# Performance work log

Measured on AMD Instinct MI355X. Metric: run time of the kernel, lower is better.

Reference implementation:

```python
import jax, jax.numpy as jnp
import numpy as np

B, N, T, E = 8, 4096, 16, 65536
D, H, O = 768, 4, 256
PER_TURN = N // T
NEG = -1e30


def setup_inputs() -> dict:
    key = jax.random.key(0)
    k = jax.random.split(key, 10)
    x = jax.random.normal(k[0], (B, N, D), dtype=jnp.float32)
    # turns sorted within each graph: node i has turn i // PER_TURN
    turns = jnp.tile(jnp.repeat(jnp.arange(T, dtype=jnp.int32), PER_TURN)[None, :], (B, 1))
    # edges: dst uniform over nodes, src uniform over nodes with turn[src] <= turn[dst]
    dst = jax.random.randint(k[1], (B, E), 0, N, dtype=jnp.int32)
    bound = (dst // PER_TURN + 1) * PER_TURN
    u = jax.random.uniform(k[2], (B, E), dtype=jnp.float32)
    src = jnp.minimum((u * bound).astype(jnp.int32), bound - 1)
    edge_index = jnp.stack([src, dst], axis=1)  # [B, 2, E]
    W = jax.random.normal(k[3], (D, H * D), dtype=jnp.float32) * 0.02
    a_src = jax.random.normal(k[4], (H, D), dtype=jnp.float32) * 0.05
    a_dst = jax.random.normal(k[5], (H, D), dtype=jnp.float32) * 0.05
    b_gat = jnp.zeros((D,), jnp.float32)
    w_att = jax.random.normal(k[6], (D, 1), dtype=jnp.float32) * 0.05
    b_att = jnp.zeros((1,), jnp.float32)
    w_cls = jax.random.normal(k[7], (D, O), dtype=jnp.float32) * 0.05
    b_cls = jnp.zeros((O,), jnp.float32)
    return dict(x=x, edge_index=edge_index, turns=turns, W=W, a_src=a_src,
                a_dst=a_dst, b_gat=b_gat, w_att=w_att, b_att=b_att,
                w_cls=w_cls, b_cls=b_cls)


def _forward(x, edge_index, turns, W, a_src, a_dst, b_gat, w_att, b_att, w_cls, b_cls, n_turns):
    n = x.shape[1]
    h_heads, d = a_src.shape

    def graph_fn(args):
        xg, ei, tg = args
        src, dst = ei[0], ei[1]

        def step(xc, t):
            active = tg <= t                                  # subgraph node mask [N]
            h = (xc @ W).reshape(n, h_heads, d)               # [N,H,D] per-head projections
            asrc = jnp.einsum('nhd,hd->nh', h, a_src)         # [N,H]
            adst = jnp.einsum('nhd,hd->nh', h, a_dst)
            emask = tg[dst] == t                              # only edges into current turn
            e = jax.nn.leaky_relu(asrc[src] + adst[dst], 0.2)  # [E,H]
            e = jnp.where(emask[:, None], e, NEG)
            # PyG GATConv add_self_loops=True: self-loop on every subgraph node
            s = jax.nn.leaky_relu(asrc + adst, 0.2)           # [N,H]
            s = jnp.where(active[:, None], s, NEG)
            m = jnp.maximum(jax.ops.segment_max(e, dst, num_segments=n), s)
            m = jnp.where(m > NEG * 0.5, m, 0.0)              # safe max for empty segments
            ee = jnp.where(emask[:, None], jnp.exp(e - m[dst]), 0.0)   # [E,H]
            se = jnp.where(active[:, None], jnp.exp(s - m), 0.0)       # [N,H]
            denom = jax.ops.segment_sum(ee, dst, num_segments=n) + se  # [N,H]
            msg = jax.ops.segment_sum(ee[:, :, None] * h[src], dst, num_segments=n)
            out = (msg + se[:, :, None] * h) / jnp.where(denom > 0, denom, 1.0)[:, :, None]
            out = out.mean(axis=1) + b_gat                    # concat=False -> mean over heads
            xn = jnp.where(active[:, None], out, xc)          # write back into graph.x
            # GlobalAttention pooling over subgraph nodes
            gate = (xn @ w_att + b_att).squeeze(-1)           # [N]
            g = jax.nn.softmax(jnp.where(active, gate, NEG))
            pooled = g @ xn                                   # [D]
            return xn, pooled @ w_cls + b_cls                 # [O]

        _, outs = jax.lax.scan(step, xg, jnp.arange(n_turns))
        return outs                                           # [T,O]

    outs = jax.lax.map(graph_fn, (x, edge_index, turns))      # sequential over graphs
    return outs[:, :, None, :]                                # [B,T,1,O] like torch.stack nesting


def reference(x, edge_index, turns, W, a_src, a_dst, b_gat, w_att, b_att, w_cls, b_cls):
    n_turns = int(turns.max()) + 1
    return _forward(x, edge_index, turns, W, a_src, a_dst, b_gat, w_att, b_att,
                    w_cls, b_cls, n_turns)
```

## Files before the change

### kernel.cpp

```cpp
#include <hip/hip_runtime.h>

typedef __attribute__((ext_vector_type(8))) short short8;
typedef __attribute__((ext_vector_type(8))) unsigned short ushort8;
typedef __attribute__((ext_vector_type(4))) float f32x4;

__device__ __forceinline__ float b2f(unsigned short u){
  union { unsigned int i; float f; } v; v.i = ((unsigned int)u)<<16; return v.f;
}
__device__ __forceinline__ unsigned short f2b(float f){
  unsigned int x = __float_as_uint(f);
  return (unsigned short)((x + 0x7fffu + ((x>>16)&1u))>>16);
}

__device__ __forceinline__ void gload16(const unsigned short* g, unsigned short* l){
  __builtin_amdgcn_global_load_lds((const __attribute__((address_space(1))) unsigned int*)g,
                                   (__attribute__((address_space(3))) unsigned int*)l, 16, 0, 0);
}

__global__ __launch_bounds__(256) void k_zero(int* p){
  p[blockIdx.x*256 + threadIdx.x] = 0;
}

__global__ __launch_bounds__(256) void k_hist(const int* __restrict__ ei, int* __restrict__ cnt){
  int idx = blockIdx.x*256 + threadIdx.x;
  int b = idx>>16, e = idx&65535;
  int dst = ei[b*131072 + 65536 + e];
  atomicAdd(&cnt[b*4096 + dst], 1);
}

__global__ __launch_bounds__(1024) void k_scan(int* __restrict__ cnt, int* __restrict__ offs){
  int b = blockIdx.x, tid = threadIdx.x;
  __shared__ int sums[1024];
  int base = tid*4;
  int c0 = cnt[b*4096+base+0], c1 = cnt[b*4096+base+1];
  int c2 = cnt[b*4096+base+2], c3 = cnt[b*4096+base+3];
  int t1 = c0, t2 = c0+c1, t3 = c0+c1+c2, tot = t3+c3;
  sums[tid] = tot;
  __syncthreads();
  for (int off=1; off<1024; off<<=1){
    int add = (tid>=off) ? sums[tid-off] : 0;
    __syncthreads();
    sums[tid] += add;
    __syncthreads();
  }
  int eb = sums[tid] - tot;
  offs[b*4097+base+0] = eb;      offs[b*4097+base+1] = eb+t1;
  offs[b*4097+base+2] = eb+t2;   offs[b*4097+base+3] = eb+t3;
  cnt[b*4096+base+0] = eb;       cnt[b*4096+base+1] = eb+t1;
  cnt[b*4096+base+2] = eb+t2;    cnt[b*4096+base+3] = eb+t3;
  if (tid==1023) offs[b*4097+4096] = sums[1023];
}

__global__ __launch_bounds__(256) void k_scatter(const int* __restrict__ ei, int* __restrict__ cur,
                                                 int* __restrict__ ss){
  int idx = blockIdx.x*256 + threadIdx.x;
  int b = idx>>16, e = idx&65535;
  int src = ei[b*131072 + e];
  int dst = ei[b*131072 + 65536 + e];
  int pos = atomicAdd(&cur[b*4096 + dst], 1);
  ss[b*65536 + pos] = src;
}

__global__ __launch_bounds__(256) void k_vavd(const float* __restrict__ W, const float* __restrict__ a_src,
                                              const float* __restrict__ a_dst, float* __restrict__ vavd){
  int wid = blockIdx.x*4 + (threadIdx.x>>6);
  int lane = threadIdx.x & 63;
  int i = wid>>3, h8 = wid&7, h = h8&3;
  const float* a = (h8<4 ? a_src : a_dst) + h*768;
  const float* wrow = W + i*3072 + h*768;
  float acc = 0.f;
  #pragma unroll
  for (int j12=0; j12<12; j12++){ int j = lane + j12*64; acc += wrow[j]*a[j]; }
  #pragma unroll
  for (int d=1; d<64; d<<=1) acc += __shfl_xor(acc, d);
  if (lane==0) vavd[i*8 + h8] = acc;
}

__global__ __launch_bounds__(256) void k_prep_w(const float* __restrict__ W, unsigned short* __restrict__ wmT,
                                                unsigned short* __restrict__ wpT){
  int g = blockIdx.x*256 + threadIdx.x;
  int i = g%768, j = g/768;
  float s = 0.f;
  #pragma unroll
  for (int h=0; h<4; h++){
    float w = W[i*3072 + h*768 + j];
    s += w;
    wpT[j*3072 + h*768 + i] = f2b(w);
  }
  wmT[j*768 + i] = f2b(0.25f*s);
}

__global__ __launch_bounds__(256) void k_prep0(const float* __restrict__ x0, const float* __restrict__ vavd,
                                               float* __restrict__ ad0){
  int b = blockIdx.y;
  int node = blockIdx.x*4 + (threadIdx.x>>6);
  int lane = threadIdx.x & 63;
  size_t roff = (size_t)(b*4096 + node)*768;
  float acc[8];
  #pragma unroll
  for (int k=0;k<8;k++) acc[k]=0.f;
  #pragma unroll
  for (int j12=0; j12<12; j12++){
    int j = lane + j12*64;
    float xv = x0[roff + j];
    const float* vp = vavd + j*8;
    #pragma unroll
    for (int k=0;k<8;k++) acc[k]+=xv*vp[k];
  }
  #pragma unroll
  for (int k=0;k<8;k++){
    #pragma unroll
    for (int d=1; d<64; d<<=1) acc[k] += __shfl_xor(acc[k], d);
  }
  if (lane==0){
    float* o = ad0 + (size_t)(b*4096 + node)*8;
    #pragma unroll
    for (int k=0;k<8;k++) o[k]=acc[k];
  }
}

__global__ __launch_bounds__(256) void k_logits(const unsigned short* __restrict__ st,
                                                const float* __restrict__ vavd, const float* __restrict__ w_att,
                                                float* __restrict__ ad, float* __restrict__ gate){
  int b = blockIdx.y;
  int node = blockIdx.x*4 + (threadIdx.x>>6);
  int lane = threadIdx.x & 63;
  size_t roff = (size_t)(b*4096 + node)*768;
  float acc[9];
  #pragma unroll
  for (int k=0;k<9;k++) acc[k]=0.f;
  #pragma unroll
  for (int j12=0; j12<12; j12++){
    int j = lane + j12*64;
    float xv = b2f(st[roff + j]);
    const float* vp = vavd + j*8;
    acc[0]+=xv*vp[0]; acc[1]+=xv*vp[1]; acc[2]+=xv*vp[2]; acc[3]+=xv*vp[3];
    acc[4]+=xv*vp[4]; acc[5]+=xv*vp[5]; acc[6]+=xv*vp[6]; acc[7]+=xv*vp[7];
    acc[8]+=xv*w_att[j];
  }
  #pragma unroll
  for (int k=0;k<9;k++){
    #pragma unroll
    for (int d=1; d<64; d<<=1) acc[k] += __shfl_xor(acc[k], d);
  }
  if (lane==0){
    float* o = ad + (size_t)(b*4096 + node)*8;
    #pragma unroll
    for (int k=0;k<8;k++) o[k]=acc[k];
    gate[b*4096 + node] = acc[8];
  }
}

__global__ __launch_bounds__(256) void k_edge(const float* __restrict__ x0, const unsigned short* __restrict__ stc,
                                              const float* __restrict__ ad, const float* __restrict__ ad0,
                                              const int* __restrict__ offs,
                                              const int* __restrict__ ssrc, unsigned short* __restrict__ zbuf, int t){
  int b = blockIdx.y, dl = blockIdx.x, tid = threadIdx.x;
  int dst = t*256 + dl;
  int lane = tid&63, wv = tid>>6;
  int e0 = offs[b*4097 + dst], e1 = offs[b*4097 + dst + 1];
  const float* adr = ad0 + (size_t)(b*4096 + dst)*8;
  float ad0_=adr[4], ad1_=adr[5], ad2_=adr[6], ad3_=adr[7];
  float sh[4];
  { float v;
    v=adr[0]+ad0_; sh[0]=v>0.f?v:0.2f*v;
    v=adr[1]+ad1_; sh[1]=v>0.f?v:0.2f*v;
    v=adr[2]+ad2_; sh[2]=v>0.f?v:0.2f*v;
    v=adr[3]+ad3_; sh[3]=v>0.f?v:0.2f*v; }
  int band = t*256;
  float mx[4] = {-1e30f,-1e30f,-1e30f,-1e30f};
  for (int i=e0+tid; i<e1; i+=256){
    int s = ssrc[b*65536 + i];
    const float* ap = (s >= band ? ad0 : ad) + (size_t)(b*4096 + s)*8;
    float v;
    v=ap[0]+ad0_; v=v>0.f?v:0.2f*v; mx[0]=fmaxf(mx[0],v);
    v=ap[1]+ad1_; v=v>0.f?v:0.2f*v; mx[1]=fmaxf(mx[1],v);
    v=ap[2]+ad2_; v=v>0.f?v:0.2f*v; mx[2]=fmaxf(mx[2],v);
    v=ap[3]+ad3_; v=v>0.f?v:0.2f*v; mx[3]=fmaxf(mx[3],v);
  }
  #pragma unroll
  for (int h=0;h<4;h++){
    #pragma unroll
    for (int d=1; d<64; d<<=1) mx[h] = fmaxf(mx[h], __shfl_xor(mx[h], d));
  }
  __shared__ float redm[4][4];
  if (lane==0){ redm[wv][0]=mx[0]; redm[wv][1]=mx[1]; redm[wv][2]=mx[2]; redm[wv][3]=mx[3]; }
  __syncthreads();
  float m[4];
  #pragma unroll
  for (int h=0;h<4;h++)
    m[h] = fmaxf(fmaxf(fmaxf(redm[0][h],redm[1][h]),fmaxf(redm[2][h],redm[3][h])), sh[h]);

  __shared__ float4 eeL[256];
  __shared__ int srcL[256];
  float den0=0.f,den1=0.f,den2=0.f,den3=0.f;
  float za[4][3] = {{0,0,0},{0,0,0},{0,0,0},{0,0,0}};
  for (int base=e0; base<e1; base+=256){
    __syncthreads();
    int i = base + tid;
    if (i < e1){
      int s = ssrc[b*65536 + i];
      const float* ap = (s >= band ? ad0 : ad) + (size_t)(b*4096 + s)*8;
      float4 wq; float v;
      v=ap[0]+ad0_; v=v>0.f?v:0.2f*v; wq.x=expf(v-m[0]); den0+=wq.x;
      v=ap[1]+ad1_; v=v>0.f?v:0.2f*v; wq.y=expf(v-m[1]); den1+=wq.y;
      v=ap[2]+ad2_; v=v>0.f?v:0.2f*v; wq.z=expf(v-m[2]); den2+=wq.z;
      v=ap[3]+ad3_; v=v>0.f?v:0.2f*v; wq.w=expf(v-m[3]); den3+=wq.w;
      eeL[tid] = wq; srcL[tid] = s;
    }
    __syncthreads();
    int cnt = e1 - base; if (cnt > 256) cnt = 256;
    for (int k=0; k<cnt; k++){
      float4 wq = eeL[k];
      int s = srcL[k];
      float xv0, xv1, xv2;
      if (s < band){
        const unsigned short* r = stc + (size_t)(b*4096 + s)*768;
        xv0=b2f(r[tid]); xv1=b2f(r[tid+256]); xv2=b2f(r[tid+512]);
      } else {
        const float* r = x0 + (size_t)(b*4096 + s)*768;
        xv0=r[tid]; xv1=r[tid+256]; xv2=r[tid+512];
      }
      za[0][0]+=wq.x*xv0; za[0][1]+=wq.x*xv1; za[0][2]+=wq.x*xv2;
      za[1][0]+=wq.y*xv0; za[1][1]+=wq.y*xv1; za[1][2]+=wq.y*xv2;
      za[2][0]+=wq.z*xv0; za[2][1]+=wq.z*xv1; za[2][2]+=wq.z*xv2;
      za[3][0]+=wq.w*xv0; za[3][1]+=wq.w*xv1; za[3][2]+=wq.w*xv2;
    }
  }
  float se[4];
  #pragma unroll
  for (int h=0;h<4;h++) se[h] = expf(sh[h]-m[h]);
  { const float* r = x0 + (size_t)(b*4096 + dst)*768;
    float xv0=r[tid], xv1=r[tid+256], xv2=r[tid+512];
    za[0][0]+=se[0]*xv0; za[0][1]+=se[0]*xv1; za[0][2]+=se[0]*xv2;
    za[1][0]+=se[1]*xv0; za[1][1]+=se[1]*xv1; za[1][2]+=se[1]*xv2;
    za[2][0]+=se[2]*xv0; za[2][1]+=se[2]*xv1; za[2][2]+=se[2]*xv2;
    za[3][0]+=se[3]*xv0; za[3][1]+=se[3]*xv1; za[3][2]+=se[3]*xv2; }
  float den[4]={den0,den1,den2,den3};
  #pragma unroll
  for (int h=0;h<4;h++){
    #pragma unroll
    for (int d=1; d<64; d<<=1) den[h] += __shfl_xor(den[h], d);
  }
  __shared__ float redd[4][4];
  if (lane==0){ redd[wv][0]=den[0]; redd[wv][1]=den[1]; redd[wv][2]=den[2]; redd[wv][3]=den[3]; }
  __syncthreads();
  unsigned short* zp = zbuf + (size_t)(b*256 + dl)*3072;
  #pragma unroll
  for (int h=0;h<4;h++){
    float dtot = redd[0][h]+redd[1][h]+redd[2][h]+redd[3][h] + se[h];
    float sc = 0.25f/dtot;
    zp[h*768 + tid      ] = f2b(za[h][0]*sc);
    zp[h*768 + tid + 256] = f2b(za[h][1]*sc);
    zp[h*768 + tid + 512] = f2b(za[h][2]*sc);
  }
}

__global__ __launch_bounds__(512) void k_mm(const unsigned short* __restrict__ zbuf,
                                            const unsigned short* __restrict__ wpT,
                                            const unsigned short* __restrict__ stc,
                                            const unsigned short* __restrict__ wmT,
                                            const float* __restrict__ bias,
                                            float* __restrict__ partA,
                                            unsigned short* __restrict__ stn, int t){
  int nwg = gridDim.x, orig = blockIdx.x;
  int cpx = nwg>>3;
  int j = (orig&7)*cpx + (orig>>3);

  int tid = threadIdx.x, lane = tid&63, w = tid>>6;
  bool jobA = j < 192;
  const unsigned short *Ap, *Bp;
  int lda, ldb, s = 0, b = 0, mrow, ncol;
  if (jobA){
    s = j/48; int q = j%48;
    mrow = (q/6)*256; ncol = (q%6)*128;
    Ap = zbuf + (size_t)mrow*3072 + s*768;  lda = 3072;
    Bp = wpT  + (size_t)ncol*3072 + s*768;  ldb = 3072;
  } else {
    int idx = j - 192; int pg = 6*t;
    b = idx/pg; int rr = idx%pg;
    mrow = (rr/6)*256; ncol = (rr%6)*128;
    Ap = stc + (size_t)b*4096*768 + (size_t)mrow*768;  lda = 768;
    Bp = wmT + (size_t)ncol*768;                       ldb = 768;
  }
  int wr = (w>>1)*64, wc = (w&1)*64;
  int lrow = lane&15, lk = (lane>>4)*8;
  __shared__ unsigned short As[3][256*32];
  __shared__ unsigned short Bs[3][128*32];
  f32x4 acc[4][4];
  #pragma unroll
  for (int m=0;m<4;m++)
    #pragma unroll
    for (int n2=0;n2<4;n2++) acc[m][n2] = (f32x4){0.f,0.f,0.f,0.f};
  int srow = w*16 + (lane>>2);
  int skb  = (lane&3)*8;
  const unsigned short* ga0 = Ap + (size_t)srow*lda + skb;
  const unsigned short* ga1 = Ap + (size_t)(128+srow)*lda + skb;
  const unsigned short* gb0 = Bp + (size_t)srow*ldb + skb;
  int lo = w*512;
  #define STAGE(bi) { gload16(ga0, &As[bi][lo]); gload16(ga1, &As[bi][4096+lo]); \
                      gload16(gb0, &Bs[bi][lo]); \
                      ga0 += 32; ga1 += 32; gb0 += 32; }
  STAGE(0)
  STAGE(1)
  #pragma unroll
  for (int kt=0; kt<24; kt++){
    int cur = kt%3;
    if (kt < 22) STAGE((kt+2)%3)
    if (kt < 22)      asm volatile("s_waitcnt vmcnt(6)" ::: "memory");
    else if (kt==22)  asm volatile("s_waitcnt vmcnt(3)" ::: "memory");
    else              asm volatile("s_waitcnt vmcnt(0)" ::: "memory");
    __builtin_amdgcn_sched_barrier(0);
    __builtin_amdgcn_s_barrier();
    __builtin_amdgcn_sched_barrier(0);
    short8 af[4], bf[4];
    #pragma unroll
    for (int m=0;m<4;m++)  af[m]  = *(const short8*)&As[cur][(wr + m*16 + lrow)*32 + lk];
    #pragma unroll
    for (int n2=0;n2<4;n2++) bf[n2] = *(const short8*)&Bs[cur][(wc + n2*16 + lrow)*32 + lk];
    __builtin_amdgcn_s_setprio(1);
    #pragma unroll
    for (int m=0;m<4;m++)
      #pragma unroll
      for (int n2=0;n2<4;n2++)
        acc[m][n2] = __builtin_amdgcn_mfma_f32_16x16x32_bf16(af[m], bf[n2], acc[m][n2], 0,0,0);
    __builtin_amdgcn_s_setprio(0);
    __builtin_amdgcn_sched_barrier(0);
    __builtin_amdgcn_s_barrier();
    __builtin_amdgcn_sched_barrier(0);
  }
  #undef STAGE
  if (jobA){
    float* op = partA + (size_t)s*2048*768;
    #pragma unroll
    for (int m=0;m<4;m++)
      #pragma unroll
      for (int n2=0;n2<4;n2++)
        #pragma unroll
        for (int r=0;r<4;r++){
          int gr = mrow + wr + m*16 + (lane>>4)*4 + r;
          int gc = ncol + wc + n2*16 + (lane&15);
          op[(size_t)gr*768 + gc] = acc[m][n2][r];
        }
  } else {
    unsigned short* cp = stn + (size_t)b*4096*768;
    #pragma unroll
    for (int m=0;m<4;m++)
      #pragma unroll
      for (int n2=0;n2<4;n2++)
        #pragma unroll
        for (int r=0;r<4;r++){
          int gr = mrow + wr + m*16 + (lane>>4)*4 + r;
          int gc = ncol + wc + n2*16 + (lane&15);
          cp[(size_t)gr*768 + gc] = f2b(acc[m][n2][r] + bias[gc]);
        }
  }
}

__global__ __launch_bounds__(256) void k_redlog(const float* __restrict__ partA, const float* __restrict__ bias,
                                                const float* __restrict__ vavd, const float* __restrict__ w_att,
                                                unsigned short* __restrict__ stn, float* __restrict__ ad,
                                                float* __restrict__ gate, int t){
  int r = blockIdx.x, tid = threadIdx.x;
  int lane = tid&63, wv = tid>>6;
  int g = r>>8;
  size_t e = (size_t)r*768;
  const size_t SL = (size_t)2048*768;
  int c0 = tid, c1 = tid+256, c2 = tid+512;
  float v0 = partA[e+c0] + partA[SL+e+c0] + partA[2*SL+e+c0] + partA[3*SL+e+c0] + bias[c0];
  float v1 = partA[e+c1] + partA[SL+e+c1] + partA[2*SL+e+c1] + partA[3*SL+e+c1] + bias[c1];
  float v2 = partA[e+c2] + partA[SL+e+c2] + partA[2*SL+e+c2] + partA[3*SL+e+c2] + bias[c2];
  size_t ro = ((size_t)g*4096 + t*256 + (r&255))*768;
  stn[ro+c0] = f2b(v0); stn[ro+c1] = f2b(v1); stn[ro+c2] = f2b(v2);
  float acc[9];
  const float *p0 = vavd + c0*8, *p1 = vavd + c1*8, *p2 = vavd + c2*8;
  #pragma unroll
  for (int k=0;k<8;k++) acc[k] = v0*p0[k] + v1*p1[k] + v2*p2[k];
  acc[8] = v0*w_att[c0] + v1*w_att[c1] + v2*w_att[c2];
  #pragma unroll
  for (int k=0;k<9;k++){
    #pragma unroll
    for (int d=1; d<64; d<<=1) acc[k] += __shfl_xor(acc[k], d);
  }
  __shared__ float red[4][9];
  if (lane==0){
    #pragma unroll
    for (int k=0;k<9;k++) red[wv][k]=acc[k];
  }
  __syncthreads();
  if (tid==0){
    size_t no = (size_t)g*4096 + t*256 + (r&255);
    float* o = ad + no*8;
    #pragma unroll
    for (int k=0;k<8;k++) o[k] = red[0][k]+red[1][k]+red[2][k]+red[3][k];
    gate[no] = red[0][8]+red[1][8]+red[2][8]+red[3][8];
  }
}

__global__ __launch_bounds__(256) void k_pool(const unsigned short* __restrict__ st, const float* __restrict__ gate,
                                              float* __restrict__ part, int t){
  int b = blockIdx.y, bx = blockIdx.x, tid = threadIdx.x;
  int lane = tid&63, wv = tid>>6;
  int A = (t+1)*256;
  const float* g = gate + b*4096;
  float mx = -1e30f;
  for (int i=tid; i<A; i+=256) mx = fmaxf(mx, g[i]);
  #pragma unroll
  for (int d=1; d<64; d<<=1) mx = fmaxf(mx, __shfl_xor(mx, d));
  __shared__ float rm[4];
  if (lane==0) rm[wv]=mx;
  __syncthreads();
  mx = fmaxf(fmaxf(rm[0],rm[1]), fmaxf(rm[2],rm[3]));
  float s = 0.f;
  for (int i=tid; i<A; i+=256) s += expf(g[i]-mx);
  #pragma unroll
  for (int d=1; d<64; d<<=1) s += __shfl_xor(s, d);
  __shared__ float rs[4];
  if (lane==0) rs[wv]=s;
  __syncthreads();
  float invS = 1.f/(rs[0]+rs[1]+rs[2]+rs[3]);
  int slice = A>>5;
  int n0 = bx*slice;
  float a0=0.f, a1=0.f, a2=0.f;
  for (int n=n0; n<n0+slice; n++){
    float wgt = expf(g[n]-mx)*invS;
    const unsigned short* r = st + (size_t)(b*4096 + n)*768;
    a0 += wgt*b2f(r[tid]); a1 += wgt*b2f(r[tid+256]); a2 += wgt*b2f(r[tid+512]);
  }
  float* p = part + (size_t)(b*32 + bx)*768;
  p[tid]=a0; p[tid+256]=a1; p[tid+512]=a2;
}

__global__ __launch_bounds__(256) void k_cls(const float* __restrict__ part, const float* __restrict__ w_cls,
                                             const float* __restrict__ b_cls, float* __restrict__ out, int t){
  int b = blockIdx.x, cg = blockIdx.y, tid = threadIdx.x;
  __shared__ float pooled[768];
  #pragma unroll
  for (int cc=0; cc<3; cc++){
    float s=0.f; int jj = tid + cc*256;
    for (int p=0; p<32; p++) s += part[(size_t)(b*32+p)*768 + jj];
    pooled[jj] = s;
  }
  __syncthreads();
  int col = tid&31, sub = tid>>5;
  int gcol = cg*32 + col;
  float s = 0.f;
  for (int jj=sub*96; jj<sub*96+96; jj++) s += pooled[jj]*w_cls[jj*256 + gcol];
  __shared__ float red[8][32];
  red[sub][col] = s;
  __syncthreads();
  if (tid < 32){
    float acc = b_cls[cg*32+tid];
    #pragma unroll
    for (int k=0;k<8;k++) acc += red[k][tid];
    out[b*4096 + t*256 + cg*32 + tid] = acc;
  }
}

extern "C" void kernel_launch(void* const* d_in, const int* in_sizes, int n_in,
                              void* d_out, int out_size, void* d_ws, size_t ws_size,
                              hipStream_t stream){
  const float* x0    = (const float*)d_in[0];
  const int*   ei    = (const int*)d_in[1];
  const float* W     = (const float*)d_in[3];
  const float* a_src = (const float*)d_in[4];
  const float* a_dst = (const float*)d_in[5];
  const float* b_gat = (const float*)d_in[6];
  const float* w_att = (const float*)d_in[7];
  const float* w_cls = (const float*)d_in[9];
  const float* b_cls = (const float*)d_in[10];
  float* out = (float*)d_out;
  char* ws = (char*)d_ws;

  size_t pos = 0;
  auto alloc = [&](size_t sz)->char*{ char* r = ws + pos; pos = (pos + sz + 255) & ~(size_t)255; return r; };
  unsigned short* st0  = (unsigned short*)alloc((size_t)8*4096*768*2);
  unsigned short* st1  = (unsigned short*)alloc((size_t)8*4096*768*2);
  unsigned short* zbuf = (unsigned short*)alloc((size_t)8*256*3072*2);
  float* adbuf = (float*)alloc((size_t)8*4096*8*4);
  float* ad0   = (float*)alloc((size_t)8*4096*8*4);
  float* gate  = (float*)alloc((size_t)8*4096*4);
  int*   ssrc  = (int*)alloc((size_t)8*65536*4);
  int*   offs  = (int*)alloc((size_t)8*4097*4);
  int*   curs  = (int*)alloc((size_t)8*4096*4);
  float* vavd  = (float*)alloc((size_t)768*8*4);
  unsigned short* wm = (unsigned short*)alloc((size_t)768*768*2);
  unsigned short* wp = (unsigned short*)alloc((size_t)768*3072*2);
  float* part  = (float*)alloc((size_t)8*32*768*4);
  float* partA = (float*)alloc((size_t)4*2048*768*4);
  unsigned short* st[2] = {st0, st1};

  k_zero   <<<128, 256, 0, stream>>>(curs);
  k_hist   <<<2048, 256, 0, stream>>>(ei, curs);
  k_scan   <<<8, 1024, 0, stream>>>(curs, offs);
  k_scatter<<<2048, 256, 0, stream>>>(ei, curs, ssrc);
  k_vavd   <<<1536, 256, 0, stream>>>(W, a_src, a_dst, vavd);
  k_prep_w <<<2304, 256, 0, stream>>>(W, wm, wp);
  k_prep0  <<<dim3(1024,8), 256, 0, stream>>>(x0, vavd, ad0);

  for (int t=0; t<16; t++){
    int cur = t&1, nxt = cur^1;
    k_edge<<<dim3(256,8), 256, 0, stream>>>(x0, st[cur], adbuf, ad0, offs, ssrc, zbuf, t);
    k_mm <<<192 + 48*t, 512, 0, stream>>>(zbuf, wp, st[cur], wm, b_gat, partA, st[nxt], t);
    k_redlog<<<2048, 256, 0, stream>>>(partA, b_gat, vavd, w_att, st[nxt], adbuf, gate, t);
    if (t >= 1)
      k_logits<<<dim3(t*64,8), 256, 0, stream>>>(st[nxt], vavd, w_att, adbuf, gate);
    k_pool<<<dim3(32,8), 256, 0, stream>>>(st[nxt], gate, part, t);
    k_cls <<<dim3(8,8), 256, 0, stream>>>(part, w_cls, b_cls, out, t);
  }
}
```

Measured before the change: 2.003 ms.

## Merge redlog and logits kernels, remap GEMM LDS staging for linear fragment reads

Result: slower. 2.180 ms (+8.8%).

```diff
diff --git a/kernel.cpp b/kernel.cpp
--- a/kernel.cpp
+++ b/kernel.cpp
@@ -116,38 +116,6 @@
     float* o = ad0 + (size_t)(b*4096 + node)*8;
     #pragma unroll
     for (int k=0;k<8;k++) o[k]=acc[k];
-  }
-}
-
-__global__ __launch_bounds__(256) void k_logits(const unsigned short* __restrict__ st,
-                                                const float* __restrict__ vavd, const float* __restrict__ w_att,
-                                                float* __restrict__ ad, float* __restrict__ gate){
-  int b = blockIdx.y;
-  int node = blockIdx.x*4 + (threadIdx.x>>6);
-  int lane = threadIdx.x & 63;
-  size_t roff = (size_t)(b*4096 + node)*768;
-  float acc[9];
-  #pragma unroll
-  for (int k=0;k<9;k++) acc[k]=0.f;
-  #pragma unroll
-  for (int j12=0; j12<12; j12++){
-    int j = lane + j12*64;
-    float xv = b2f(st[roff + j]);
-    const float* vp = vavd + j*8;
-    acc[0]+=xv*vp[0]; acc[1]+=xv*vp[1]; acc[2]+=xv*vp[2]; acc[3]+=xv*vp[3];
-    acc[4]+=xv*vp[4]; acc[5]+=xv*vp[5]; acc[6]+=xv*vp[6]; acc[7]+=xv*vp[7];
-    acc[8]+=xv*w_att[j];
-  }
-  #pragma unroll
-  for (int k=0;k<9;k++){
-    #pragma unroll
-    for (int d=1; d<64; d<<=1) acc[k] += __shfl_xor(acc[k], d);
-  }
-  if (lane==0){
-    float* o = ad + (size_t)(b*4096 + node)*8;
-    #pragma unroll
-    for (int k=0;k<8;k++) o[k]=acc[k];
-    gate[b*4096 + node] = acc[8];
   }
 }
 
@@ -284,7 +252,6 @@
     Bp = wmT + (size_t)ncol*768;                       ldb = 768;
   }
   int wr = (w>>1)*64, wc = (w&1)*64;
-  int lrow = lane&15, lk = (lane>>4)*8;
   __shared__ unsigned short As[3][256*32];
   __shared__ unsigned short Bs[3][128*32];
   f32x4 acc[4][4];
@@ -292,8 +259,8 @@
   for (int m=0;m<4;m++)
     #pragma unroll
     for (int n2=0;n2<4;n2++) acc[m][n2] = (f32x4){0.f,0.f,0.f,0.f};
-  int srow = w*16 + (lane>>2);
-  int skb  = (lane&3)*8;
+  int srow = w*16 + (lane&15);
+  int skb  = (lane>>4)*8;
   const unsigned short* ga0 = Ap + (size_t)srow*lda + skb;
   const unsigned short* ga1 = Ap + (size_t)(128+srow)*lda + skb;
   const unsigned short* gb0 = Bp + (size_t)srow*ldb + skb;
@@ -303,6 +270,8 @@
                       ga0 += 32; ga1 += 32; gb0 += 32; }
   STAGE(0)
   STAGE(1)
+  int aoff0 = ((wr>>4))*512 + lane*8;
+  int boff0 = ((wc>>4))*512 + lane*8;
   #pragma unroll
   for (int kt=0; kt<24; kt++){
     int cur = kt%3;
@@ -315,9 +284,9 @@
     __builtin_amdgcn_sched_barrier(0);
     short8 af[4], bf[4];
     #pragma unroll
-    for (int m=0;m<4;m++)  af[m]  = *(const short8*)&As[cur][(wr + m*16 + lrow)*32 + lk];
-    #pragma unroll
-    for (int n2=0;n2<4;n2++) bf[n2] = *(const short8*)&Bs[cur][(wc + n2*16 + lrow)*32 + lk];
+    for (int m=0;m<4;m++)  af[m]  = *(const short8*)&As[cur][aoff0 + m*512];
+    #pragma unroll
+    for (int n2=0;n2<4;n2++) bf[n2] = *(const short8*)&Bs[cur][boff0 + n2*512];
     __builtin_amdgcn_s_setprio(1);
     #pragma unroll
     for (int m=0;m<4;m++)
@@ -357,43 +326,76 @@
   }
 }
 
-__global__ __launch_bounds__(256) void k_redlog(const float* __restrict__ partA, const float* __restrict__ bias,
-                                                const float* __restrict__ vavd, const float* __restrict__ w_att,
-                                                unsigned short* __restrict__ stn, float* __restrict__ ad,
-                                                float* __restrict__ gate, int t){
-  int r = blockIdx.x, tid = threadIdx.x;
+__global__ __launch_bounds__(256) void k_post(const float* __restrict__ partA, const float* __restrict__ bias,
+                                              const float* __restrict__ vavd, const float* __restrict__ w_att,
+                                              const unsigned short* __restrict__ st,
+                                              unsigned short* __restrict__ stn, float* __restrict__ ad,
+                                              float* __restrict__ gate, int t){
+  int j = blockIdx.x, tid = threadIdx.x;
   int lane = tid&63, wv = tid>>6;
-  int g = r>>8;
-  size_t e = (size_t)r*768;
-  const size_t SL = (size_t)2048*768;
-  int c0 = tid, c1 = tid+256, c2 = tid+512;
-  float v0 = partA[e+c0] + partA[SL+e+c0] + partA[2*SL+e+c0] + partA[3*SL+e+c0] + bias[c0];
-  float v1 = partA[e+c1] + partA[SL+e+c1] + partA[2*SL+e+c1] + partA[3*SL+e+c1] + bias[c1];
-  float v2 = partA[e+c2] + partA[SL+e+c2] + partA[2*SL+e+c2] + partA[3*SL+e+c2] + bias[c2];
-  size_t ro = ((size_t)g*4096 + t*256 + (r&255))*768;
-  stn[ro+c0] = f2b(v0); stn[ro+c1] = f2b(v1); stn[ro+c2] = f2b(v2);
-  float acc[9];
-  const float *p0 = vavd + c0*8, *p1 = vavd + c1*8, *p2 = vavd + c2*8;
-  #pragma unroll
-  for (int k=0;k<8;k++) acc[k] = v0*p0[k] + v1*p1[k] + v2*p2[k];
-  acc[8] = v0*w_att[c0] + v1*w_att[c1] + v2*w_att[c2];
-  #pragma unroll
-  for (int k=0;k<9;k++){
-    #pragma unroll
-    for (int d=1; d<64; d<<=1) acc[k] += __shfl_xor(acc[k], d);
-  }
-  __shared__ float red[4][9];
-  if (lane==0){
-    #pragma unroll
-    for (int k=0;k<9;k++) red[wv][k]=acc[k];
-  }
-  __syncthreads();
-  if (tid==0){
-    size_t no = (size_t)g*4096 + t*256 + (r&255);
-    float* o = ad + no*8;
-    #pragma unroll
-    for (int k=0;k<8;k++) o[k] = red[0][k]+red[1][k]+red[2][k]+red[3][k];
-    gate[no] = red[0][8]+red[1][8]+red[2][8]+red[3][8];
+  if (j < 2048){
+    int r = j;
+    int g = r>>8;
+    size_t e = (size_t)r*768;
+    const size_t SL = (size_t)2048*768;
+    int c0 = tid, c1 = tid+256, c2 = tid+512;
+    float v0 = partA[e+c0] + partA[SL+e+c0] + partA[2*SL+e+c0] + partA[3*SL+e+c0] + bias[c0];
+    float v1 = partA[e+c1] + partA[SL+e+c1] + partA[2*SL+e+c1] + partA[3*SL+e+c1] + bias[c1];
+    float v2 = partA[e+c2] + partA[SL+e+c2] + partA[2*SL+e+c2] + partA[3*SL+e+c2] + bias[c2];
+    size_t ro = ((size_t)g*4096 + t*256 + (r&255))*768;
+    stn[ro+c0] = f2b(v0); stn[ro+c1] = f2b(v1); stn[ro+c2] = f2b(v2);
+    float acc[9];
+    const float *p0 = vavd + c0*8, *p1 = vavd + c1*8, *p2 = vavd + c2*8;
+    #pragma unroll
+    for (int k=0;k<8;k++) acc[k] = v0*p0[k] + v1*p1[k] + v2*p2[k];
+    acc[8] = v0*w_att[c0] + v1*w_att[c1] + v2*w_att[c2];
+    #pragma unroll
+    for (int k=0;k<9;k++){
+      #pragma unroll
+      for (int d=1; d<64; d<<=1) acc[k] += __shfl_xor(acc[k], d);
+    }
+    __shared__ float red[4][9];
+    if (lane==0){
+      #pragma unroll
+      for (int k=0;k<9;k++) red[wv][k]=acc[k];
+    }
+    __syncthreads();
+    if (tid==0){
+      size_t no = (size_t)g*4096 + t*256 + (r&255);
+      float* o = ad + no*8;
+      #pragma unroll
+      for (int k=0;k<8;k++) o[k] = red[0][k]+red[1][k]+red[2][k]+red[3][k];
+      gate[no] = red[0][8]+red[1][8]+red[2][8]+red[3][8];
+    }
+  } else {
+    int idx = j - 2048;
+    int per = t*64;
+    int b = idx/per;
+    int node = (idx%per)*4 + (tid>>6);
+    size_t roff = (size_t)(b*4096 + node)*768;
+    float acc[9];
+    #pragma unroll
+    for (int k=0;k<9;k++) acc[k]=0.f;
+    #pragma unroll
+    for (int j12=0; j12<12; j12++){
+      int jj = lane + j12*64;
+      float xv = b2f(st[roff + jj]);
+      const float* vp = vavd + jj*8;
+      acc[0]+=xv*vp[0]; acc[1]+=xv*vp[1]; acc[2]+=xv*vp[2]; acc[3]+=xv*vp[3];
+      acc[4]+=xv*vp[4]; acc[5]+=xv*vp[5]; acc[6]+=xv*vp[6]; acc[7]+=xv*vp[7];
+      acc[8]+=xv*w_att[jj];
+    }
+    #pragma unroll
+    for (int k=0;k<9;k++){
+      #pragma unroll
+      for (int d=1; d<64; d<<=1) acc[k] += __shfl_xor(acc[k], d);
+    }
+    if (lane==0){
+      float* o = ad + (size_t)(b*4096 + node)*8;
+      #pragma unroll
+      for (int k=0;k<8;k++) o[k]=acc[k];
+      gate[b*4096 + node] = acc[8];
+    }
   }
 }
 
@@ -502,9 +504,7 @@
     int cur = t&1, nxt = cur^1;
     k_edge<<<dim3(256,8), 256, 0, stream>>>(x0, st[cur], adbuf, ad0, offs, ssrc, zbuf, t);
     k_mm <<<192 + 48*t, 512, 0, stream>>>(zbuf, wp, st[cur], wm, b_gat, partA, st[nxt], t);
-    k_redlog<<<2048, 256, 0, stream>>>(partA, b_gat, vavd, w_att, st[nxt], adbuf, gate, t);
-    if (t >= 1)
-      k_logits<<<dim3(t*64,8), 256, 0, stream>>>(st[nxt], vavd, w_att, adbuf, gate);
+    k_post<<<2048 + t*512, 256, 0, stream>>>(partA, b_gat, vavd, w_att, st[nxt], st[nxt], adbuf, gate, t);
     k_pool<<<dim3(32,8), 256, 0, stream>>>(st[nxt], gate, part, t);
     k_cls <<<dim3(8,8), 256, 0, stream>>>(part, w_cls, b_cls, out, t);
   }
```
